# Kernel optimization log

Measured on AMD Instinct MI355X. Metric: run time of the kernel, lower is better.

## Reference

```python
import jax, jax.numpy as jnp
import numpy as np

N_NODES = 100000
N_EDGES = 3200000


def gcn_conv(x, edge_index, W, b, n_nodes):
    # PyG GCNConv: x' = D^{-1/2} (A + I) D^{-1/2} (x W) + b
    h = x @ W  # [N, C_out]
    loop = jnp.arange(n_nodes, dtype=edge_index.dtype)
    src = jnp.concatenate([edge_index[0], loop])  # source nodes j
    dst = jnp.concatenate([edge_index[1], loop])  # target nodes i (aggregation)
    deg = jax.ops.segment_sum(jnp.ones_like(dst, h.dtype), dst, num_segments=n_nodes)
    dinv = jnp.where(deg > 0, jax.lax.rsqrt(deg), 0.0)
    norm = dinv[src] * dinv[dst]  # [E+N]
    msg = h[src] * norm[:, None]  # gather + scale
    out = jax.ops.segment_sum(msg, dst, num_segments=n_nodes)  # scatter-add
    return out + b


def setup_inputs() -> dict:
    key = jax.random.key(0)
    ks = jax.random.split(key, 6)
    x = jax.random.normal(ks[0], (N_NODES, 1), dtype=jnp.float32)
    edge_index = jax.random.randint(ks[1], (2, N_EDGES), 0, N_NODES, dtype=jnp.int64)
    W1 = jax.random.normal(ks[2], (1, 16), dtype=jnp.float32) * (1.0 / np.sqrt(1))
    b1 = jnp.zeros((16,), dtype=jnp.float32)
    W2 = jax.random.normal(ks[3], (16, 16), dtype=jnp.float32) * (1.0 / np.sqrt(16))
    b2 = jnp.zeros((16,), dtype=jnp.float32)
    Wl = jax.random.normal(ks[4], (16, 1), dtype=jnp.float32) * (1.0 / np.sqrt(16))
    bl = jnp.zeros((1,), dtype=jnp.float32)
    return {"x": x, "edge_index": edge_index, "W1": W1, "b1": b1,
            "W2": W2, "b2": b2, "Wl": Wl, "bl": bl}


def reference(x, edge_index, W1, b1, W2, b2, Wl, bl):
    n = x.shape[0]
    h = gcn_conv(x, edge_index, W1, b1, n)
    h = jax.nn.relu(h)
    # F.dropout(training=self.training): identity in eval mode
    h = gcn_conv(h, edge_index, W2, b2, n)
    return h @ Wl + bl  # [N, 1]
```

## Files before the change

### kernel.cpp

```cpp
#include <hip/hip_runtime.h>

#define N_NODES  100000
#define N_EDGES  3200000
#define NB       8
#define BN       12544
#define SUBS     96
#define GRID     (NB * SUBS)
#define THR      512
#define SLICE    33336
#define CAP_BLK  5120


__global__ __launch_bounds__(THR, 6) void k_degpart(
        const int* __restrict__ src, const int* __restrict__ dstp,
        unsigned* __restrict__ cnt, unsigned* __restrict__ pedge,
        float* __restrict__ partials) {
    __shared__ float facc[BN];
    __shared__ unsigned cur;
    const int tid = threadIdx.x, lane = tid & 63;
    const int bu = blockIdx.x / SUBS, sub = blockIdx.x % SUBS;
    for (int i = tid; i < BN; i += THR) facc[i] = 0.f;
    if (tid == 0) cur = 0;
    __syncthreads();

    const unsigned base_node = (unsigned)bu * BN;
    unsigned* reg = pedge + (size_t)blockIdx.x * CAP_BLK;
    const uint4* s4 = (const uint4*)src;
    const uint4* d4 = (const uint4*)dstp;
    const int e0 = sub * SLICE;
    const int qbeg = e0 >> 2;
    const int qlim = (e0 + SLICE < N_EDGES ? e0 + SLICE : N_EDGES) >> 2;

    for (int q = qbeg + tid; q < qlim; q += THR) {
        const uint4 dv = d4[q], sv = s4[q];
        const unsigned dd[4] = { dv.x, dv.y, dv.z, dv.w };
        const unsigned ss[4] = { sv.x, sv.y, sv.z, sv.w };
        #pragma unroll
        for (int k = 0; k < 4; ++k) {
            const unsigned d = dd[k];
            const unsigned dl = d - base_node;
            const bool in = (d / BN) == (unsigned)bu;
            if (in) atomicAdd(&facc[dl], 1.f);
            const unsigned long long m = __ballot(in);
            const unsigned pos = (unsigned)__popcll(m & ((1ull << lane) - 1ull));
            unsigned b0 = 0;
            if (lane == 0) b0 = atomicAdd(&cur, (unsigned)__popcll(m));
            b0 = __shfl(b0, 0, 64);
            if (in) {
                const unsigned slot = b0 + pos;
                if (slot < CAP_BLK) reg[slot] = ss[k] | (dl << 17);
            }
        }
    }
    __syncthreads();
    if (tid == 0) cnt[blockIdx.x] = cur < CAP_BLK ? cur : CAP_BLK;
    float* po = partials + (size_t)blockIdx.x * BN;
    for (int i = tid; i < BN; i += THR) po[i] = facc[i];
}

__global__ __launch_bounds__(THR, 6) void k_acc(
        const unsigned* __restrict__ pedge, const unsigned* __restrict__ cnt,
        const float* __restrict__ vals, float* __restrict__ partials) {
    __shared__ float facc[BN];
    const int tid = threadIdx.x;
    for (int i = tid; i < BN; i += THR) facc[i] = 0.f;
    __syncthreads();
    const unsigned n = cnt[blockIdx.x];
    const unsigned* reg = pedge + (size_t)blockIdx.x * CAP_BLK;
    for (unsigned j = tid; j < n; j += THR) {
        const unsigned w = reg[j];
        atomicAdd(&facc[w >> 17], vals[w & 0x1FFFFu]);
    }
    __syncthreads();
    float* po = partials + (size_t)blockIdx.x * BN;
    for (int i = tid; i < BN; i += THR) po[i] = facc[i];
}

__device__ __forceinline__ float sum_partials(const float* __restrict__ partials,
                                              int g) {
    const int bu = g / BN, l = g - bu * BN;
    const float* pp = partials + (size_t)(bu * SUBS) * BN + l;
    float s = 0.f;
    #pragma unroll 16
    for (int k = 0; k < SUBS; ++k) s += pp[(size_t)k * BN];
    return s;
}

__global__ __launch_bounds__(THR) void k_red1(const float* __restrict__ x,
        const float* __restrict__ partials, float* __restrict__ dinv,
        float* __restrict__ xs) {
    const int g = blockIdx.x * THR + threadIdx.x;
    if (g >= N_NODES) return;
    const float deg = 1.f + sum_partials(partials, g);
    const float di = rsqrtf(deg);
    dinv[g] = di;
    xs[g] = x[g] * di;
}

__global__ __launch_bounds__(THR) void k_red2(const float* __restrict__ x,
        const float* __restrict__ partials, const float* __restrict__ dinv,
        const float* __restrict__ W1, const float* __restrict__ b1,
        const float* __restrict__ W2, const float* __restrict__ Wl,
        float* __restrict__ us, float* __restrict__ uself) {
    const int g = blockIdx.x * THR + threadIdx.x;
    if (g >= N_NODES) return;
    const float sum = sum_partials(partials, g);
    const float di = dinv[g];
    const float s1 = di * sum + x[g] * di * di;
    float u = 0.f;
    #pragma unroll
    for (int c = 0; c < 16; ++c) {
        float vcc = 0.f;
        #pragma unroll
        for (int k = 0; k < 16; ++k) vcc += W2[c * 16 + k] * Wl[k];
        u += fmaxf(W1[c] * s1 + b1[c], 0.f) * vcc;
    }
    us[g] = u * di;
    uself[g] = u * di * di;
}

__global__ __launch_bounds__(THR) void k_red3(const float* __restrict__ partials,
        const float* __restrict__ dinv, const float* __restrict__ uself,
        const float* __restrict__ W2, const float* __restrict__ b2,
        const float* __restrict__ Wl, const float* __restrict__ bl,
        float* __restrict__ out) {
    const int g = blockIdx.x * THR + threadIdx.x;
    if (g >= N_NODES) return;
    const float sum = sum_partials(partials, g);
    float vcb = bl[0];
    #pragma unroll
    for (int c = 0; c < 16; ++c) {
        float vcc = 0.f;
        #pragma unroll
        for (int k = 0; k < 16; ++k) vcc += W2[c * 16 + k] * Wl[k];
        vcb += b2[c] * vcc;
    }
    out[g] = dinv[g] * sum + uself[g] + vcb;
}

extern "C" void kernel_launch(void* const* d_in, const int* in_sizes, int n_in,
                              void* d_out, int out_size, void* d_ws, size_t ws_size,
                              hipStream_t stream) {
    const float* x  = (const float*)d_in[0];
    const int*   ei = (const int*)d_in[1];
    const float* W1 = (const float*)d_in[2];
    const float* b1 = (const float*)d_in[3];
    const float* W2 = (const float*)d_in[4];
    const float* b2 = (const float*)d_in[5];
    const float* Wl = (const float*)d_in[6];
    const float* bl = (const float*)d_in[7];
    float* out = (float*)d_out;

    const int* src  = ei;
    const int* dstp = ei + N_EDGES;

    unsigned* cnt      = (unsigned*)d_ws;
    unsigned* pedge    = cnt + 1024;
    float*    partials = (float*)(pedge + (size_t)GRID * CAP_BLK);
    float*    dinv     = partials + (size_t)GRID * BN;
    float*    xs       = dinv + N_NODES;
    float*    us       = xs + N_NODES;
    float*    uself    = us + N_NODES;

    const int red_blocks = (N_NODES + THR - 1) / THR;

    k_degpart<<<GRID, THR, 0, stream>>>(src, dstp, cnt, pedge, partials);
    k_red1<<<red_blocks, THR, 0, stream>>>(x, partials, dinv, xs);
    k_acc<<<GRID, THR, 0, stream>>>(pedge, cnt, xs, partials);
    k_red2<<<red_blocks, THR, 0, stream>>>(x, partials, dinv, W1, b1, W2, Wl, us, uself);
    k_acc<<<GRID, THR, 0, stream>>>(pedge, cnt, us, partials);
    k_red3<<<red_blocks, THR, 0, stream>>>(partials, dinv, uself, W2, b2, Wl, bl, out);
}
```

Before: 188.2 us.

## Build CSR by destination and replace partial-sum atomics with per-node segment gather

Degree counting now uses 16-bit per-sub-block counts, which an exclusive scan turns into per-node offsets. A placement kernel then scatters source ids into a dst-sorted CSR layout. The two aggregation passes become per-node loops that gather the source values directly. This drops the 96-way float partial-sum buffers and the two shared-atomic accumulation passes, at the cost of an extra prefix kernel and a placement pass. Per-thread variable-length loops may load-balance poorly and read csr uncoalesced.

```diff
diff --git a/kernel.cpp b/kernel.cpp
--- a/kernel.cpp
+++ b/kernel.cpp
@@ -9,17 +9,17 @@
 #define THR      512
 #define SLICE    33336
 #define CAP_BLK  5120
-
+#define CAP_B    440000
 
 __global__ __launch_bounds__(THR, 6) void k_degpart(
         const int* __restrict__ src, const int* __restrict__ dstp,
         unsigned* __restrict__ cnt, unsigned* __restrict__ pedge,
-        float* __restrict__ partials) {
-    __shared__ float facc[BN];
+        unsigned short* __restrict__ cnt16) {
+    __shared__ unsigned facc[BN];
     __shared__ unsigned cur;
     const int tid = threadIdx.x, lane = tid & 63;
     const int bu = blockIdx.x / SUBS, sub = blockIdx.x % SUBS;
-    for (int i = tid; i < BN; i += THR) facc[i] = 0.f;
+    for (int i = tid; i < BN; i += THR) facc[i] = 0u;
     if (tid == 0) cur = 0;
     __syncthreads();
 
@@ -40,7 +40,7 @@
             const unsigned d = dd[k];
             const unsigned dl = d - base_node;
             const bool in = (d / BN) == (unsigned)bu;
-            if (in) atomicAdd(&facc[dl], 1.f);
+            if (in) atomicAdd(&facc[dl], 1u);
             const unsigned long long m = __ballot(in);
             const unsigned pos = (unsigned)__popcll(m & ((1ull << lane) - 1ull));
             unsigned b0 = 0;
@@ -54,57 +54,102 @@
     }
     __syncthreads();
     if (tid == 0) cnt[blockIdx.x] = cur < CAP_BLK ? cur : CAP_BLK;
-    float* po = partials + (size_t)blockIdx.x * BN;
-    for (int i = tid; i < BN; i += THR) po[i] = facc[i];
-}
-
-__global__ __launch_bounds__(THR, 6) void k_acc(
+    unsigned short* po = cnt16 + (size_t)blockIdx.x * BN;
+    for (int i = tid; i < BN; i += THR) po[i] = (unsigned short)facc[i];
+}
+
+__global__ __launch_bounds__(THR) void k_red1x(const float* __restrict__ x,
+        unsigned short* __restrict__ cnt16, unsigned* __restrict__ deg,
+        float* __restrict__ dinv, float* __restrict__ xs) {
+    const int g = blockIdx.x * THR + threadIdx.x;
+    if (g >= N_NODES) return;
+    const int bu = g / BN, l = g - bu * BN;
+    unsigned short* pp = cnt16 + (size_t)(bu * SUBS) * BN + l;
+    unsigned run = 0;
+    #pragma unroll 8
+    for (int s = 0; s < SUBS; ++s) {
+        const unsigned c = pp[(size_t)s * BN];
+        pp[(size_t)s * BN] = (unsigned short)run;
+        run += c;
+    }
+    deg[g] = run;
+    const float di = rsqrtf((float)run + 1.f);
+    dinv[g] = di;
+    xs[g] = x[g] * di;
+}
+
+__global__ __launch_bounds__(1024) void k_prefix(const unsigned* __restrict__ deg,
+        unsigned* __restrict__ nodeOff, unsigned* __restrict__ absOff) {
+    __shared__ unsigned wtot[16];
+    __shared__ unsigned ctot, carry;
+    const int bu = blockIdx.x;
+    const int tid = threadIdx.x, wave = tid >> 6, lane = tid & 63;
+    if (tid == 0) carry = 0;
+    __syncthreads();
+    for (int c = 0; c < 13; ++c) {
+        const int l = c * 1024 + tid;
+        const int g = bu * BN + l;
+        unsigned v = (l < BN && g < N_NODES) ? deg[g] : 0u;
+        unsigned ps = v;
+        #pragma unroll
+        for (int d = 1; d < 64; d <<= 1) {
+            unsigned o = __shfl_up(ps, d, 64);
+            if (lane >= d) ps += o;
+        }
+        if (lane == 63) wtot[wave] = ps;
+        __syncthreads();
+        if (tid == 0) {
+            unsigned run = 0;
+            #pragma unroll
+            for (int w = 0; w < 16; ++w) { unsigned t = wtot[w]; wtot[w] = run; run += t; }
+            ctot = run;
+        }
+        __syncthreads();
+        const unsigned excl = carry + wtot[wave] + (ps - v);
+        if (l < BN) {
+            nodeOff[bu * BN + l] = excl;
+            if (g < N_NODES) absOff[g] = (unsigned)bu * CAP_B + excl;
+        }
+        __syncthreads();
+        if (tid == 0) carry += ctot;
+        __syncthreads();
+    }
+}
+
+__global__ __launch_bounds__(THR, 3) void k_place(
         const unsigned* __restrict__ pedge, const unsigned* __restrict__ cnt,
-        const float* __restrict__ vals, float* __restrict__ partials) {
-    __shared__ float facc[BN];
+        const unsigned short* __restrict__ cnt16, const unsigned* __restrict__ nodeOff,
+        unsigned* __restrict__ csr) {
+    __shared__ unsigned curs[BN];
     const int tid = threadIdx.x;
-    for (int i = tid; i < BN; i += THR) facc[i] = 0.f;
-    __syncthreads();
-    const unsigned n = cnt[blockIdx.x];
-    const unsigned* reg = pedge + (size_t)blockIdx.x * CAP_BLK;
+    const int r = blockIdx.x;
+    const int bu = r / SUBS;
+    const unsigned short* sp = cnt16 + (size_t)r * BN;
+    const unsigned* no = nodeOff + bu * BN;
+    for (int i = tid; i < BN; i += THR) curs[i] = no[i] + (unsigned)sp[i];
+    __syncthreads();
+    const unsigned n = cnt[r];
+    const unsigned* reg = pedge + (size_t)r * CAP_BLK;
+    unsigned* cb = csr + (size_t)bu * CAP_B;
     for (unsigned j = tid; j < n; j += THR) {
         const unsigned w = reg[j];
-        atomicAdd(&facc[w >> 17], vals[w & 0x1FFFFu]);
-    }
-    __syncthreads();
-    float* po = partials + (size_t)blockIdx.x * BN;
-    for (int i = tid; i < BN; i += THR) po[i] = facc[i];
-}
-
-__device__ __forceinline__ float sum_partials(const float* __restrict__ partials,
-                                              int g) {
-    const int bu = g / BN, l = g - bu * BN;
-    const float* pp = partials + (size_t)(bu * SUBS) * BN + l;
-    float s = 0.f;
-    #pragma unroll 16
-    for (int k = 0; k < SUBS; ++k) s += pp[(size_t)k * BN];
-    return s;
-}
-
-__global__ __launch_bounds__(THR) void k_red1(const float* __restrict__ x,
-        const float* __restrict__ partials, float* __restrict__ dinv,
-        float* __restrict__ xs) {
-    const int g = blockIdx.x * THR + threadIdx.x;
-    if (g >= N_NODES) return;
-    const float deg = 1.f + sum_partials(partials, g);
-    const float di = rsqrtf(deg);
-    dinv[g] = di;
-    xs[g] = x[g] * di;
-}
-
-__global__ __launch_bounds__(THR) void k_red2(const float* __restrict__ x,
-        const float* __restrict__ partials, const float* __restrict__ dinv,
+        const unsigned slot = atomicAdd(&curs[w >> 17], 1u);
+        cb[slot] = w & 0x1FFFFu;
+    }
+}
+
+__global__ __launch_bounds__(THR) void k_seg2(const float* __restrict__ x,
+        const float* __restrict__ xs, const unsigned* __restrict__ csr,
+        const unsigned* __restrict__ absOff, const unsigned* __restrict__ deg,
+        const float* __restrict__ dinv,
         const float* __restrict__ W1, const float* __restrict__ b1,
         const float* __restrict__ W2, const float* __restrict__ Wl,
         float* __restrict__ us, float* __restrict__ uself) {
     const int g = blockIdx.x * THR + threadIdx.x;
     if (g >= N_NODES) return;
-    const float sum = sum_partials(partials, g);
+    const unsigned o = absOff[g], d = deg[g];
+    float sum = 0.f;
+    for (unsigned k = 0; k < d; ++k) sum += xs[csr[o + k]];
     const float di = dinv[g];
     const float s1 = di * sum + x[g] * di * di;
     float u = 0.f;
@@ -119,14 +164,18 @@
     uself[g] = u * di * di;
 }
 
-__global__ __launch_bounds__(THR) void k_red3(const float* __restrict__ partials,
-        const float* __restrict__ dinv, const float* __restrict__ uself,
+__global__ __launch_bounds__(THR) void k_seg3(const unsigned* __restrict__ csr,
+        const unsigned* __restrict__ absOff, const unsigned* __restrict__ deg,
+        const float* __restrict__ us, const float* __restrict__ dinv,
+        const float* __restrict__ uself,
         const float* __restrict__ W2, const float* __restrict__ b2,
         const float* __restrict__ Wl, const float* __restrict__ bl,
         float* __restrict__ out) {
     const int g = blockIdx.x * THR + threadIdx.x;
     if (g >= N_NODES) return;
-    const float sum = sum_partials(partials, g);
+    const unsigned o = absOff[g], d = deg[g];
+    float sum = 0.f;
+    for (unsigned k = 0; k < d; ++k) sum += us[csr[o + k]];
     float vcb = bl[0];
     #pragma unroll
     for (int c = 0; c < 16; ++c) {
@@ -154,20 +203,26 @@
     const int* src  = ei;
     const int* dstp = ei + N_EDGES;
 
-    unsigned* cnt      = (unsigned*)d_ws;
-    unsigned* pedge    = cnt + 1024;
-    float*    partials = (float*)(pedge + (size_t)GRID * CAP_BLK);
-    float*    dinv     = partials + (size_t)GRID * BN;
-    float*    xs       = dinv + N_NODES;
-    float*    us       = xs + N_NODES;
-    float*    uself    = us + N_NODES;
+    unsigned* cnt         = (unsigned*)d_ws;
+    unsigned* pedge       = cnt + 1024;
+    unsigned short* cnt16 = (unsigned short*)(pedge + (size_t)GRID * CAP_BLK);
+    unsigned* nodeOff     = (unsigned*)(cnt16 + (size_t)GRID * BN);
+    unsigned* absOff      = nodeOff + NB * BN;
+    unsigned* deg         = absOff + N_NODES;
+    float*    dinv        = (float*)(deg + N_NODES);
+    float*    xs          = dinv + N_NODES;
+    float*    us          = xs + N_NODES;
+    float*    uself       = us + N_NODES;
+    unsigned* csr         = (unsigned*)(uself + N_NODES);
 
     const int red_blocks = (N_NODES + THR - 1) / THR;
 
-    k_degpart<<<GRID, THR, 0, stream>>>(src, dstp, cnt, pedge, partials);
-    k_red1<<<red_blocks, THR, 0, stream>>>(x, partials, dinv, xs);
-    k_acc<<<GRID, THR, 0, stream>>>(pedge, cnt, xs, partials);
-    k_red2<<<red_blocks, THR, 0, stream>>>(x, partials, dinv, W1, b1, W2, Wl, us, uself);
-    k_acc<<<GRID, THR, 0, stream>>>(pedge, cnt, us, partials);
-    k_red3<<<red_blocks, THR, 0, stream>>>(partials, dinv, uself, W2, b2, Wl, bl, out);
-}
+    k_degpart<<<GRID, THR, 0, stream>>>(src, dstp, cnt, pedge, cnt16);
+    k_red1x<<<red_blocks, THR, 0, stream>>>(x, cnt16, deg, dinv, xs);
+    k_prefix<<<NB, 1024, 0, stream>>>(deg, nodeOff, absOff);
+    k_place<<<GRID, THR, 0, stream>>>(pedge, cnt, cnt16, nodeOff, csr);
+    k_seg2<<<red_blocks, THR, 0, stream>>>(x, xs, csr, absOff, deg, dinv,
+                                           W1, b1, W2, Wl, us, uself);
+    k_seg3<<<red_blocks, THR, 0, stream>>>(csr, absOff, deg, us, dinv, uself,
+                                           W2, b2, Wl, bl, out);
+}
```

Result: slower. 238.8 us (+26.9%).

## Store degree partials as uint16 and merge edge regions in fewer accumulation blocks

Applied to the files above, without the earlier changes.

Degree counting now uses integer shared atomics and writes per-block partial counts as 16-bit values, which halves the partial-buffer traffic for the first reduction. The accumulation kernel now has each 1024-thread block process three edge regions, so there are 32 partial slices per node bucket instead of 96. That cuts the partial writes and the reduction reads in the later reduction kernels. In exchange there are fewer blocks, so less parallelism, and each block does more serial shared-memory atomic work.

```diff
diff --git a/kernel.cpp b/kernel.cpp
--- a/kernel.cpp
+++ b/kernel.cpp
@@ -4,9 +4,13 @@
 #define N_EDGES  3200000
 #define NB       8
 #define BN       12544
-#define SUBS     96
-#define GRID     (NB * SUBS)
+#define S1       96
+#define G1       (NB * S1)
+#define SA       32
+#define GA       (NB * SA)
+#define RPB      (S1 / SA)
 #define THR      512
+#define THRA     1024
 #define SLICE    33336
 #define CAP_BLK  5120
 
@@ -14,12 +18,12 @@
 __global__ __launch_bounds__(THR, 6) void k_degpart(
         const int* __restrict__ src, const int* __restrict__ dstp,
         unsigned* __restrict__ cnt, unsigned* __restrict__ pedge,
-        float* __restrict__ partials) {
-    __shared__ float facc[BN];
+        unsigned short* __restrict__ cnt16) {
+    __shared__ unsigned facc[BN];
     __shared__ unsigned cur;
     const int tid = threadIdx.x, lane = tid & 63;
-    const int bu = blockIdx.x / SUBS, sub = blockIdx.x % SUBS;
-    for (int i = tid; i < BN; i += THR) facc[i] = 0.f;
+    const int bu = blockIdx.x / S1, sub = blockIdx.x % S1;
+    for (int i = tid; i < BN; i += THR) facc[i] = 0u;
     if (tid == 0) cur = 0;
     __syncthreads();
 
@@ -40,7 +44,7 @@
             const unsigned d = dd[k];
             const unsigned dl = d - base_node;
             const bool in = (d / BN) == (unsigned)bu;
-            if (in) atomicAdd(&facc[dl], 1.f);
+            if (in) atomicAdd(&facc[dl], 1u);
             const unsigned long long m = __ballot(in);
             const unsigned pos = (unsigned)__popcll(m & ((1ull << lane) - 1ull));
             unsigned b0 = 0;
@@ -54,47 +58,56 @@
     }
     __syncthreads();
     if (tid == 0) cnt[blockIdx.x] = cur < CAP_BLK ? cur : CAP_BLK;
-    float* po = partials + (size_t)blockIdx.x * BN;
-    for (int i = tid; i < BN; i += THR) po[i] = facc[i];
+    unsigned short* po = cnt16 + (size_t)blockIdx.x * BN;
+    for (int i = tid; i < BN; i += THR) po[i] = (unsigned short)facc[i];
 }
 
-__global__ __launch_bounds__(THR, 6) void k_acc(
+__global__ __launch_bounds__(THR) void k_red1(const float* __restrict__ x,
+        const unsigned short* __restrict__ cnt16,
+        float* __restrict__ dinv, float* __restrict__ xs) {
+    const int g = blockIdx.x * THR + threadIdx.x;
+    if (g >= N_NODES) return;
+    const int bu = g / BN, l = g - bu * BN;
+    const unsigned short* pp = cnt16 + (size_t)(bu * S1) * BN + l;
+    unsigned run = 0;
+    #pragma unroll 8
+    for (int s = 0; s < S1; ++s) run += pp[(size_t)s * BN];
+    const float di = rsqrtf((float)run + 1.f);
+    dinv[g] = di;
+    xs[g] = x[g] * di;
+}
+
+__global__ __launch_bounds__(THRA) void k_acc(
         const unsigned* __restrict__ pedge, const unsigned* __restrict__ cnt,
         const float* __restrict__ vals, float* __restrict__ partials) {
     __shared__ float facc[BN];
     const int tid = threadIdx.x;
-    for (int i = tid; i < BN; i += THR) facc[i] = 0.f;
+    const int bu = blockIdx.x / SA, sub = blockIdx.x % SA;
+    for (int i = tid; i < BN; i += THRA) facc[i] = 0.f;
     __syncthreads();
-    const unsigned n = cnt[blockIdx.x];
-    const unsigned* reg = pedge + (size_t)blockIdx.x * CAP_BLK;
-    for (unsigned j = tid; j < n; j += THR) {
-        const unsigned w = reg[j];
-        atomicAdd(&facc[w >> 17], vals[w & 0x1FFFFu]);
+    #pragma unroll
+    for (int r3 = 0; r3 < RPB; ++r3) {
+        const int r = bu * S1 + sub * RPB + r3;
+        const unsigned n = cnt[r];
+        const unsigned* reg = pedge + (size_t)r * CAP_BLK;
+        for (unsigned j = tid; j < n; j += THRA) {
+            const unsigned w = reg[j];
+            atomicAdd(&facc[w >> 17], vals[w & 0x1FFFFu]);
+        }
     }
     __syncthreads();
     float* po = partials + (size_t)blockIdx.x * BN;
-    for (int i = tid; i < BN; i += THR) po[i] = facc[i];
+    for (int i = tid; i < BN; i += THRA) po[i] = facc[i];
 }
 
 __device__ __forceinline__ float sum_partials(const float* __restrict__ partials,
                                               int g) {
     const int bu = g / BN, l = g - bu * BN;
-    const float* pp = partials + (size_t)(bu * SUBS) * BN + l;
+    const float* pp = partials + (size_t)(bu * SA) * BN + l;
     float s = 0.f;
-    #pragma unroll 16
-    for (int k = 0; k < SUBS; ++k) s += pp[(size_t)k * BN];
+    #pragma unroll
+    for (int k = 0; k < SA; ++k) s += pp[(size_t)k * BN];
     return s;
-}
-
-__global__ __launch_bounds__(THR) void k_red1(const float* __restrict__ x,
-        const float* __restrict__ partials, float* __restrict__ dinv,
-        float* __restrict__ xs) {
-    const int g = blockIdx.x * THR + threadIdx.x;
-    if (g >= N_NODES) return;
-    const float deg = 1.f + sum_partials(partials, g);
-    const float di = rsqrtf(deg);
-    dinv[g] = di;
-    xs[g] = x[g] * di;
 }
 
 __global__ __launch_bounds__(THR) void k_red2(const float* __restrict__ x,
@@ -154,20 +167,21 @@
     const int* src  = ei;
     const int* dstp = ei + N_EDGES;
 
-    unsigned* cnt      = (unsigned*)d_ws;
-    unsigned* pedge    = cnt + 1024;
-    float*    partials = (float*)(pedge + (size_t)GRID * CAP_BLK);
-    float*    dinv     = partials + (size_t)GRID * BN;
-    float*    xs       = dinv + N_NODES;
-    float*    us       = xs + N_NODES;
-    float*    uself    = us + N_NODES;
+    unsigned* cnt         = (unsigned*)d_ws;
+    unsigned* pedge       = cnt + 1024;
+    unsigned short* cnt16 = (unsigned short*)(pedge + (size_t)G1 * CAP_BLK);
+    float*    partials    = (float*)(cnt16 + (size_t)G1 * BN);
+    float*    dinv        = partials + (size_t)GA * BN;
+    float*    xs          = dinv + N_NODES;
+    float*    us          = xs + N_NODES;
+    float*    uself       = us + N_NODES;
 
     const int red_blocks = (N_NODES + THR - 1) / THR;
 
-    k_degpart<<<GRID, THR, 0, stream>>>(src, dstp, cnt, pedge, partials);
-    k_red1<<<red_blocks, THR, 0, stream>>>(x, partials, dinv, xs);
-    k_acc<<<GRID, THR, 0, stream>>>(pedge, cnt, xs, partials);
+    k_degpart<<<G1, THR, 0, stream>>>(src, dstp, cnt, pedge, cnt16);
+    k_red1<<<red_blocks, THR, 0, stream>>>(x, cnt16, dinv, xs);
+    k_acc<<<GA, THRA, 0, stream>>>(pedge, cnt, xs, partials);
     k_red2<<<red_blocks, THR, 0, stream>>>(x, partials, dinv, W1, b1, W2, Wl, us, uself);
-    k_acc<<<GRID, THR, 0, stream>>>(pedge, cnt, us, partials);
+    k_acc<<<GA, THRA, 0, stream>>>(pedge, cnt, us, partials);
     k_red3<<<red_blocks, THR, 0, stream>>>(partials, dinv, uself, W2, b2, Wl, bl, out);
 }
```

Measured after the change: 172.6 us. 8.3% less time.
